# Optimization experiments

Hardware: AMD Instinct MI355X
Metric: run time of the kernel (lower is better)

Reference implementation:

```python
import jax, jax.numpy as jnp
import numpy as np


def setup_inputs() -> dict:
    key = jax.random.key(0)
    k1, k2 = jax.random.split(key)
    B, C, H, W = 8, 128, 256, 256
    K = 1024
    img = jax.random.normal(k1, (B, C, H, W), dtype=jnp.float32)
    spx = jax.random.randint(k2, (B, H, W), 0, K, dtype=jnp.int32)
    return {"img": img, "spx": spx, "K": K}


def reference(img, spx, K):
    # Superpixel max-pooling: for each batch and channel, take the max of img
    # over all pixels sharing the same superpixel label. Output [B, C, K].
    B, C, H, W = img.shape
    x = img.reshape(B, C, H * W).transpose(0, 2, 1)   # [B, HW, C]
    seg = spx.reshape(B, H * W)                       # [B, HW]
    # segment_max reduces over the leading axis; vmap over batch.
    pooled = jax.vmap(
        lambda xf, s: jax.ops.segment_max(xf, s, num_segments=K)
    )(x, seg)                                         # [B, K, C]
    return pooled.transpose(0, 2, 1)                  # [B, C, K]
```

## Files before the change

### kernel.cpp

```cpp
#include <hip/hip_runtime.h>


#define NTHREADS 1024

constexpr int B_ = 8, C_ = 128, H_ = 256, W_ = 256, K_ = 1024;
constexpr int HW_ = H_ * W_;
constexpr int CSUB = 2;
constexpr int CGRP = C_ / CSUB;
constexpr int STRIDE = CSUB + 1;

__device__ __forceinline__ unsigned f2o(float f) {
    unsigned u = __float_as_uint(f);
    return u ^ (unsigned)(((int)u >> 31) | (int)0x80000000);
}
__device__ __forceinline__ float o2f(unsigned o) {
    return __uint_as_float(o ^ (((int)o >= 0) ? 0xFFFFFFFFu : 0x80000000u));
}

__global__ __launch_bounds__(NTHREADS) void SupPixPool_25366076850473_kernel(
    const float* __restrict__ img, const int* __restrict__ spx, float* __restrict__ out)
{
    __shared__ unsigned smax[K_ * STRIDE];
    const int tid = threadIdx.x;

    for (int i = tid; i < K_ * STRIDE; i += NTHREADS)
        smax[i] = 0x007FFFFFu;
    __syncthreads();

    const int b  = blockIdx.x / CGRP;
    const int cg = blockIdx.x % CGRP;
    const int c0 = cg * CSUB;

    const int4*  lab4 = (const int4*)(spx + (size_t)b * HW_);
    const float* imgb = img + ((size_t)(b * C_ + c0)) * HW_;
    constexpr int NV = HW_ / 4;

    for (int v = tid; v < NV; v += NTHREADS) {
        int4 lab = lab4[v];
        int a0 = lab.x * STRIDE, a1 = lab.y * STRIDE,
            a2 = lab.z * STRIDE, a3 = lab.w * STRIDE;
#pragma unroll
        for (int c = 0; c < CSUB; ++c) {
            float4 x = ((const float4*)(imgb + (size_t)c * HW_))[v];
            atomicMax(&smax[a0 + c], f2o(x.x));
            atomicMax(&smax[a1 + c], f2o(x.y));
            atomicMax(&smax[a2 + c], f2o(x.z));
            atomicMax(&smax[a3 + c], f2o(x.w));
        }
    }
    __syncthreads();

    float* outb = out + ((size_t)(b * C_ + c0)) * K_;
    for (int i = tid; i < K_ * CSUB; i += NTHREADS) {
        int c = i >> 10;
        int k = i & (K_ - 1);
        outb[c * K_ + k] = o2f(smax[k * STRIDE + c]);
    }
}

extern "C" void kernel_launch(void* const* d_in, const int* in_sizes, int n_in,
                              void* d_out, int out_size, void* d_ws, size_t ws_size,
                              hipStream_t stream) {
    const float* img = (const float*)d_in[0];
    const int*   spx = (const int*)d_in[1];
    float*       out = (float*)d_out;
    dim3 grid(B_ * CGRP);
    hipLaunchKernelGGL(SupPixPool_25366076850473_kernel, grid, dim3(NTHREADS), 0, stream,
                       img, spx, out);
}
```

Before: 358.9 us.

## Filter LDS atomics by pre-checking current max and compacting survivors per wave

After the first iteration, each thread reads the current per-segment maxima for both channels and keeps only candidates that exceed them. Survivors are compacted through a per-wave LDS queue using ballot and popcount, then drained 64 at a time as dense atomicMax batches. The aim is to remove the many LDS atomics that would not change the stored value. The cost is extra LDS reads, ballots and queue traffic, and the padded stride of 3 becomes a stride of 2 so each pair can be read as one uint2, which may bring back bank conflicts.

After: 366.8 us. 1.02x slower.

```diff
diff --git a/kernel.cpp b/kernel.cpp
--- a/kernel.cpp
+++ b/kernel.cpp
@@ -7,7 +7,9 @@
 constexpr int HW_ = H_ * W_;
 constexpr int CSUB = 2;
 constexpr int CGRP = C_ / CSUB;
-constexpr int STRIDE = CSUB + 1;
+constexpr int STRIDE = 2;
+constexpr int NWAVES = NTHREADS / 64;
+constexpr int QCAP = 256;
 
 __device__ __forceinline__ unsigned f2o(float f) {
     unsigned u = __float_as_uint(f);
@@ -21,7 +23,10 @@
     const float* __restrict__ img, const int* __restrict__ spx, float* __restrict__ out)
 {
     __shared__ unsigned smax[K_ * STRIDE];
-    const int tid = threadIdx.x;
+    __shared__ unsigned long long q[NWAVES * QCAP];
+    const int tid = threadIdx.x, lane = tid & 63, wid = tid >> 6;
+    const int qbase = wid * QCAP;
+    const unsigned long long lmask = (1ull << lane) - 1ull;
 
     for (int i = tid; i < K_ * STRIDE; i += NTHREADS)
         smax[i] = 0x007FFFFFu;
@@ -31,22 +36,59 @@
     const int cg = blockIdx.x % CGRP;
     const int c0 = cg * CSUB;
 
-    const int4*  lab4 = (const int4*)(spx + (size_t)b * HW_);
-    const float* imgb = img + ((size_t)(b * C_ + c0)) * HW_;
+    const int4*   lab4 = (const int4*)(spx + (size_t)b * HW_);
+    const float4* img0 = (const float4*)(img + ((size_t)(b * C_ + c0)) * HW_);
+    const float4* img1 = (const float4*)(img + ((size_t)(b * C_ + c0 + 1)) * HW_);
     constexpr int NV = HW_ / 4;
 
-    for (int v = tid; v < NV; v += NTHREADS) {
+    int qcount = 0;
+
+    for (int v = tid, it = 0; v < NV; v += NTHREADS, ++it) {
         int4 lab = lab4[v];
-        int a0 = lab.x * STRIDE, a1 = lab.y * STRIDE,
-            a2 = lab.z * STRIDE, a3 = lab.w * STRIDE;
+        float4 x0 = img0[v], x1 = img1[v];
+        int a[4] = { lab.x * STRIDE, lab.y * STRIDE, lab.z * STRIDE, lab.w * STRIDE };
+        unsigned o[8] = { f2o(x0.x), f2o(x0.y), f2o(x0.z), f2o(x0.w),
+                          f2o(x1.x), f2o(x1.y), f2o(x1.z), f2o(x1.w) };
+        if (it == 0) {
 #pragma unroll
-        for (int c = 0; c < CSUB; ++c) {
-            float4 x = ((const float4*)(imgb + (size_t)c * HW_))[v];
-            atomicMax(&smax[a0 + c], f2o(x.x));
-            atomicMax(&smax[a1 + c], f2o(x.y));
-            atomicMax(&smax[a2 + c], f2o(x.z));
-            atomicMax(&smax[a3 + c], f2o(x.w));
+            for (int j = 0; j < 4; ++j) {
+                atomicMax(&smax[a[j]],     o[j]);
+                atomicMax(&smax[a[j] + 1], o[j + 4]);
+            }
+        } else {
+            uint2 cur[4];
+#pragma unroll
+            for (int j = 0; j < 4; ++j)
+                cur[j] = *(const uint2*)&smax[a[j]];
+#pragma unroll
+            for (int j = 0; j < 8; ++j) {
+                int aj = a[j & 3] + (j >> 2);
+                unsigned cj = (j < 4) ? cur[j & 3].x : cur[j & 3].y;
+                bool pass = o[j] > cj;
+                unsigned long long m = __ballot(pass);
+                if (m) {
+                    int cnt = __popcll(m);
+                    if (qcount + cnt <= QCAP) {
+                        if (pass) {
+                            int pos = qbase + qcount + __popcll(m & lmask);
+                            q[pos] = ((unsigned long long)o[j] << 32) | (unsigned)aj;
+                        }
+                        qcount += cnt;
+                    } else {
+                        if (pass) atomicMax(&smax[aj], o[j]);
+                    }
+                }
+            }
+            while (qcount >= 64) {
+                qcount -= 64;
+                unsigned long long e = q[qbase + qcount + lane];
+                atomicMax(&smax[(unsigned)(e & 0xFFFFFFFFu)], (unsigned)(e >> 32));
+            }
         }
+    }
+    if (lane < qcount) {
+        unsigned long long e = q[qbase + lane];
+        atomicMax(&smax[(unsigned)(e & 0xFFFFFFFFu)], (unsigned)(e >> 32));
     }
     __syncthreads();
 
```
